# Kernel optimization log

Hardware: AMD Instinct MI355X
Metric: run time of the kernel (lower is better)

## Reference

```python
import jax, jax.numpy as jnp
import numpy as np

N_NODES = 100000
N_EDGES = 1600000
F_IN = 128
H1 = 128
H2 = 128
N_CLASSES = 40


def setup_inputs() -> dict:
    key = jax.random.key(0)
    ks = jax.random.split(key, 8)
    node_features = jax.random.normal(ks[0], (N_NODES, F_IN), dtype=jnp.float32)
    edge_indices = jax.random.randint(ks[1], (2, N_EDGES), 0, N_NODES, dtype=jnp.int32)
    # Glorot-ish init for weights
    W1 = jax.random.normal(ks[2], (F_IN, H1), dtype=jnp.float32) / np.sqrt(F_IN)
    b1 = jnp.zeros((H1,), dtype=jnp.float32)
    W2 = jax.random.normal(ks[3], (H1, H2), dtype=jnp.float32) / np.sqrt(H1)
    b2 = jnp.zeros((H2,), dtype=jnp.float32)
    Wl = jax.random.normal(ks[4], (H2, N_CLASSES), dtype=jnp.float32) / np.sqrt(H2)
    bl = jnp.zeros((N_CLASSES,), dtype=jnp.float32)
    return {
        "node_features": node_features,
        "edge_indices": edge_indices,
        "W1": W1, "b1": b1,
        "W2": W2, "b2": b2,
        "Wl": Wl, "bl": bl,
    }


def _gcn_norm(edge_indices, n_nodes):
    # PyG GCNConv default: add self-loops, symmetric normalization.
    src = jnp.concatenate([edge_indices[0], jnp.arange(n_nodes, dtype=edge_indices.dtype)])
    dst = jnp.concatenate([edge_indices[1], jnp.arange(n_nodes, dtype=edge_indices.dtype)])
    deg = jax.ops.segment_sum(jnp.ones_like(dst, dtype=jnp.float32), dst,
                              num_segments=n_nodes)  # degree over destinations (col)
    deg_inv_sqrt = jnp.where(deg > 0, jax.lax.rsqrt(deg), 0.0)
    norm = deg_inv_sqrt[src] * deg_inv_sqrt[dst]  # (E + N,)
    return src, dst, norm


def _gcn_conv(x, W, b, src, dst, norm, n_nodes):
    xw = x @ W                                    # (N, F_out) dense GEMM
    msg = xw[src] * norm[:, None]                 # gather + scale: (E+N, F_out)
    out = jax.ops.segment_sum(msg, dst, num_segments=n_nodes)  # scatter-add
    return out + b


def reference(node_features, edge_indices, W1, b1, W2, b2, Wl, bl):
    n = node_features.shape[0]
    src, dst, norm = _gcn_norm(edge_indices, n)
    # dropout is identity in eval mode
    x = jax.nn.relu(_gcn_conv(node_features, W1, b1, src, dst, norm, n))
    x = jax.nn.relu(_gcn_conv(x, W2, b2, src, dst, norm, n))
    return x @ Wl + bl  # (N, num_classes)
```

## Files before the change

### kernel.cpp

```cpp
#include <hip/hip_runtime.h>


typedef unsigned int uint32;
typedef unsigned short u16;

#define FD 128

using short8 = __attribute__((ext_vector_type(8))) short;
using f32x4  = __attribute__((ext_vector_type(4))) float;

union U4S8 { uint4 u; short8 s; };

__device__ __forceinline__ u16 f2bf(float f) {
    uint32 u = __float_as_uint(f);
    uint32 r = ((u >> 16) & 1u) + 0x7FFFu;
    return (u16)((u + r) >> 16);
}
__device__ __forceinline__ float bf2f(u16 s) { return __uint_as_float((uint32)s << 16); }
__device__ __forceinline__ float bfLo(uint32 w) { return __uint_as_float(w << 16); }
__device__ __forceinline__ float bfHi(uint32 w) { return __uint_as_float(w & 0xFFFF0000u); }

__global__ void k_beacon(float* __restrict__ out, long long n, float val) {
    long long i = (long long)blockIdx.x * 256 + threadIdx.x;
    if (i < n) out[i] = val;
}

__global__ __launch_bounds__(256) void k_count(const int* __restrict__ dst,
                                               int* __restrict__ cnt,
                                               int* __restrict__ rank,
                                               int ne, int nn) {
    long long base = ((long long)blockIdx.x * 256 + threadIdx.x) * 4;
    if (base + 4 <= (long long)ne) {
        int4 d4 = *(const int4*)(dst + base);
        int a0 = ((unsigned)d4.x < (unsigned)nn) ? d4.x : nn;
        int a1 = ((unsigned)d4.y < (unsigned)nn) ? d4.y : nn;
        int a2 = ((unsigned)d4.z < (unsigned)nn) ? d4.z : nn;
        int a3 = ((unsigned)d4.w < (unsigned)nn) ? d4.w : nn;
        int4 r4;
        r4.x = atomicAdd(&cnt[a0], 1);
        r4.y = atomicAdd(&cnt[a1], 1);
        r4.z = atomicAdd(&cnt[a2], 1);
        r4.w = atomicAdd(&cnt[a3], 1);
        *(int4*)(rank + base) = r4;
    } else {
        for (long long e = base; e < (long long)ne; e++) {
            int d = dst[e];
            int a = ((unsigned)d < (unsigned)nn) ? d : nn;
            rank[e] = atomicAdd(&cnt[a], 1);
        }
    }
}

__global__ void k_scan_a(const int* __restrict__ cnt, int* __restrict__ row_start,
                         int* __restrict__ bsum, float* __restrict__ dis, int nn) {
    __shared__ int tmp[256];
    int t = threadIdx.x;
    int i = blockIdx.x * 256 + t;
    int v = (i < nn) ? cnt[i] : 0;
    if (i < nn) dis[i] = rsqrtf((float)(v + 1));
    tmp[t] = v;
    __syncthreads();
    for (int off = 1; off < 256; off <<= 1) {
        int x = (t >= off) ? tmp[t - off] : 0;
        __syncthreads();
        tmp[t] += x;
        __syncthreads();
    }
    if (i < nn) row_start[i] = tmp[t] - v;
    if (t == 255) bsum[blockIdx.x] = tmp[255];
}

__global__ void k_scan_b(int* bsum, int nb) {
    __shared__ int tmp[512];
    __shared__ int carry;
    int t = threadIdx.x;
    if (t == 0) carry = 0;
    __syncthreads();
    for (int base = 0; base < nb; base += 512) {
        int i = base + t;
        int v = (i < nb) ? bsum[i] : 0;
        tmp[t] = v;
        __syncthreads();
        for (int off = 1; off < 512; off <<= 1) {
            int x = (t >= off) ? tmp[t - off] : 0;
            __syncthreads();
            tmp[t] += x;
            __syncthreads();
        }
        if (i < nb) bsum[i] = tmp[t] - v + carry;
        __syncthreads();
        if (t == 0) carry += tmp[511];
        __syncthreads();
    }
}

__global__ void k_scan_c(int* __restrict__ row_start, const int* __restrict__ bsum,
                         int nn, int ne) {
    int i = blockIdx.x * 256 + threadIdx.x;
    if (i < nn) row_start[i] += bsum[blockIdx.x];
    if (i == 0) row_start[nn] = ne;
}

__global__ __launch_bounds__(256) void k_fill_mgemm(
    const float* __restrict__ A, const float* __restrict__ W,
    uint32* __restrict__ yt, const float* __restrict__ rowscale, int M,
    const int* __restrict__ src, const int* __restrict__ dst,
    const int* __restrict__ rank, const int* __restrict__ row_start,
    int* __restrict__ col_idx, int ne, int nn,
    int nfill, int ngemm) {
    __shared__ uint4 Bf[4][8][64];

    int bid = blockIdx.x;
    int both2 = 2 * (nfill < ngemm ? nfill : ngemm);
    bool isfill;
    int idx;
    if (bid < both2) { isfill = (bid & 1) == 0; idx = bid >> 1; }
    else { isfill = nfill > ngemm; idx = (both2 >> 1) + (bid - both2); }

    int t = threadIdx.x;

    if (isfill) {
        long long base = ((long long)idx * 256 + t) * 4;
        if (base + 4 <= (long long)ne) {
            int4 d4 = *(const int4*)(dst + base);
            int4 s4 = *(const int4*)(src + base);
            int4 r4 = *(const int4*)(rank + base);
            int dd[4] = {d4.x, d4.y, d4.z, d4.w};
            int ss[4] = {s4.x, s4.y, s4.z, s4.w};
            int rr[4] = {r4.x, r4.y, r4.z, r4.w};
            int pp[4];
#pragma unroll
            for (int r = 0; r < 4; r++) {
                bool ok = (unsigned)dd[r] < (unsigned)nn;
                int dv = ok ? dd[r] : 0;
                int p = row_start[dv] + rr[r];
                pp[r] = ok ? p : -1;
            }
#pragma unroll
            for (int r = 0; r < 4; r++)
                if ((unsigned)pp[r] < (unsigned)ne) col_idx[pp[r]] = ss[r];
        } else {
            for (long long e = base; e < (long long)ne; e++) {
                int d = dst[e];
                if ((unsigned)d >= (unsigned)nn) continue;
                int p = row_start[d] + rank[e];
                if ((unsigned)p < (unsigned)ne) col_idx[p] = src[e];
            }
        }
        return;
    }

    for (int e = t; e < 4 * 8 * 64; e += 256) {
        int kc = e / (8 * 64);
        int rem = e - kc * (8 * 64);
        int ct = rem >> 6;
        int l  = rem & 63;
        int k0 = kc * 32 + (l >> 4) * 8;
        int c  = ct * 16 + (l & 15);
        u16 us[8];
#pragma unroll
        for (int i = 0; i < 8; i++) us[i] = f2bf(W[(size_t)(k0 + i) * 128 + c]);
        uint4 u;
        u.x = (uint32)us[0] | ((uint32)us[1] << 16);
        u.y = (uint32)us[2] | ((uint32)us[3] << 16);
        u.z = (uint32)us[4] | ((uint32)us[5] << 16);
        u.w = (uint32)us[6] | ((uint32)us[7] << 16);
        Bf[kc][ct][l] = u;
    }
    __syncthreads();

    int lane = t & 63, wv = t >> 6;
    int r0 = idx * 64 + wv * 16;
    if (r0 >= M) return;

    int arow = r0 + (lane & 15);
    if (arow >= M) arow = M - 1;
    U4S8 af[4];
#pragma unroll
    for (int kc = 0; kc < 4; kc++) {
        const float4* s = (const float4*)(A + (size_t)arow * FD + kc * 32 + (lane >> 4) * 8);
        float4 v0 = s[0], v1 = s[1];
        uint4 u;
        u.x = (uint32)f2bf(v0.x) | ((uint32)f2bf(v0.y) << 16);
        u.y = (uint32)f2bf(v0.z) | ((uint32)f2bf(v0.w) << 16);
        u.z = (uint32)f2bf(v1.x) | ((uint32)f2bf(v1.y) << 16);
        u.w = (uint32)f2bf(v1.z) | ((uint32)f2bf(v1.w) << 16);
        af[kc].u = u;
    }

    f32x4 acc[8];
#pragma unroll
    for (int ct = 0; ct < 8; ct++) acc[ct] = f32x4{0.f, 0.f, 0.f, 0.f};
#pragma unroll
    for (int kc = 0; kc < 4; kc++) {
#pragma unroll
        for (int ct = 0; ct < 8; ct++) {
            U4S8 b;
            b.u = Bf[kc][ct][lane];
            acc[ct] = __builtin_amdgcn_mfma_f32_16x16x32_bf16(af[kc].s, b.s, acc[ct], 0, 0, 0);
        }
    }

    int rb = r0 + (lane >> 4) * 4;
#pragma unroll
    for (int r = 0; r < 4; r++) {
        int row = rb + r;
        int rc = row < M ? row : M - 1;
        float rs = rowscale[rc];
#pragma unroll
        for (int ct = 0; ct < 8; ct++) {
            float v = acc[ct][r] * rs;
            float vn = __shfl_xor(v, 1);
            if (!(lane & 1) && row < M) {
                uint32 word = (uint32)f2bf(v) | ((uint32)f2bf(vn) << 16);
                yt[(size_t)row * 128 + (ct * 16 + (lane & 15)) / 2] = word;
            }
        }
    }
}

template <int NOUT, bool INBF, bool OUTBF>
__global__ __launch_bounds__(256) void k_mgemm(const void* __restrict__ Ap,
                                               const float* __restrict__ W,
                                               void* __restrict__ out,
                                               const float* __restrict__ bias,
                                               const float* __restrict__ rowscale,
                                               int M) {
    constexpr int NT = (NOUT + 15) / 16;
    __shared__ uint4 Bf[4][NT][64];

    int t = threadIdx.x;
    for (int e = t; e < 4 * NT * 64; e += 256) {
        int kc = e / (NT * 64);
        int rem = e - kc * (NT * 64);
        int ct = rem >> 6;
        int l  = rem & 63;
        int k0 = kc * 32 + (l >> 4) * 8;
        int c  = ct * 16 + (l & 15);
        u16 us[8];
#pragma unroll
        for (int i = 0; i < 8; i++)
            us[i] = (c < NOUT) ? f2bf(W[(size_t)(k0 + i) * NOUT + c]) : (u16)0;
        uint4 u;
        u.x = (uint32)us[0] | ((uint32)us[1] << 16);
        u.y = (uint32)us[2] | ((uint32)us[3] << 16);
        u.z = (uint32)us[4] | ((uint32)us[5] << 16);
        u.w = (uint32)us[6] | ((uint32)us[7] << 16);
        Bf[kc][ct][l] = u;
    }
    __syncthreads();

    int lane = t & 63, wv = t >> 6;
    int r0 = blockIdx.x * 64 + wv * 16;
    if (r0 >= M) return;

    int arow = r0 + (lane & 15);
    if (arow >= M) arow = M - 1;
    U4S8 af[4];
    if (INBF) {
        const u16* A = (const u16*)Ap;
#pragma unroll
        for (int kc = 0; kc < 4; kc++)
            af[kc].u = *(const uint4*)(A + (size_t)arow * FD + kc * 32 + (lane >> 4) * 8);
    } else {
        const float* A = (const float*)Ap;
#pragma unroll
        for (int kc = 0; kc < 4; kc++) {
            const float4* s = (const float4*)(A + (size_t)arow * FD + kc * 32 + (lane >> 4) * 8);
            float4 v0 = s[0], v1 = s[1];
            uint4 u;
            u.x = (uint32)f2bf(v0.x) | ((uint32)f2bf(v0.y) << 16);
            u.y = (uint32)f2bf(v0.z) | ((uint32)f2bf(v0.w) << 16);
            u.z = (uint32)f2bf(v1.x) | ((uint32)f2bf(v1.y) << 16);
            u.w = (uint32)f2bf(v1.z) | ((uint32)f2bf(v1.w) << 16);
            af[kc].u = u;
        }
    }

    f32x4 acc[NT];
#pragma unroll
    for (int ct = 0; ct < NT; ct++) acc[ct] = f32x4{0.f, 0.f, 0.f, 0.f};
#pragma unroll
    for (int kc = 0; kc < 4; kc++) {
#pragma unroll
        for (int ct = 0; ct < NT; ct++) {
            U4S8 b;
            b.u = Bf[kc][ct][lane];
            acc[ct] = __builtin_amdgcn_mfma_f32_16x16x32_bf16(af[kc].s, b.s, acc[ct], 0, 0, 0);
        }
    }

    int rb = r0 + (lane >> 4) * 4;
    if (OUTBF) {
        uint32* yt = (uint32*)out;
#pragma unroll
        for (int r = 0; r < 4; r++) {
            int row = rb + r;
            int rc = row < M ? row : M - 1;
            float rs = rowscale ? rowscale[rc] : 1.f;
#pragma unroll
            for (int ct = 0; ct < NT; ct++) {
                float v = acc[ct][r] * rs;
                float vn = __shfl_xor(v, 1);
                if (!(lane & 1) && row < M) {
                    uint32 word = (uint32)f2bf(v) | ((uint32)f2bf(vn) << 16);
                    yt[(size_t)row * 128 + (ct * 16 + (lane & 15)) / 2] = word;
                }
            }
        }
    } else {
        float* fo = (float*)out;
#pragma unroll
        for (int r = 0; r < 4; r++) {
            int row = rb + r;
            if (row >= M) continue;
#pragma unroll
            for (int ct = 0; ct < NT; ct++) {
                int c = ct * 16 + (lane & 15);
                if (c < NOUT) {
                    float v = acc[ct][r];
                    if (bias) v += bias[c];
                    fo[(size_t)row * NOUT + c] = v;
                }
            }
        }
    }
}

__global__ __launch_bounds__(256) void k_agg(const uint32* __restrict__ yt,
                                             const float* __restrict__ dis,
                                             const int* __restrict__ row_start,
                                             const int* __restrict__ col_idx,
                                             const float* __restrict__ bias,
                                             uint32* __restrict__ outp,
                                             int nn, int ne) {
    int lane = threadIdx.x & 63;
    int wid  = threadIdx.x >> 6;
    int g    = lane >> 4;
    int sub  = lane & 15;

    float2 bq[4];
#pragma unroll
    for (int k = 0; k < 4; k++) bq[k] = *(const float2*)(bias + (sub * 4 + k) * 2);

    const int stride = gridDim.x * 16;
    for (int n0 = blockIdx.x * 16 + wid * 4; n0 < nn; n0 += stride) {
        int n = n0 + g;
        bool act = n < nn;
        int nl = act ? n : 0;

        float di = dis[nl];
        int jb = row_start[nl];
        int je = row_start[nl + 1];
        if (!act) { jb = 0; je = 0; }
        if (jb < 0) jb = 0;
        if (je > ne) je = ne;
        int deg = je - jb; if (deg < 0) deg = 0;
        int je1 = je - 1;

        uint4 sv = *(const uint4*)(yt + (size_t)nl * 128 + sub * 4);
        float a0 = bfLo(sv.x), a1 = bfHi(sv.x);
        float a2 = bfLo(sv.y), a3 = bfHi(sv.y);
        float a4 = bfLo(sv.z), a5 = bfHi(sv.z);
        float a6 = bfLo(sv.w), a7 = bfHi(sv.w);

        int m = deg;
        m = max(m, __shfl_xor(m, 16));
        m = max(m, __shfl_xor(m, 32));

        for (int base = 0; base < m; base += 8) {
            int jj = jb + base + (sub & 7);
            int jc = jj < je ? jj : je1;
            if (jc < 0) jc = 0;
            int sl = col_idx[jc];
            if ((unsigned)sl >= (unsigned)nn) sl = -1;

            int ss[8];
            float ww[8];
#pragma unroll
            for (int r = 0; r < 8; r++) {
                int s = __shfl(sl, (lane & 48) + r);
                ww[r] = (base + r < deg && s >= 0) ? 1.f : 0.f;
                ss[r] = s >= 0 ? s : 0;
            }
            uint4 uu[8];
#pragma unroll
            for (int r = 0; r < 8; r++)
                uu[r] = *(const uint4*)(yt + (size_t)ss[r] * 128 + sub * 4);
#pragma unroll
            for (int r = 0; r < 8; r++) {
                float wg = ww[r];
                a0 = fmaf(bfLo(uu[r].x), wg, a0); a1 = fmaf(bfHi(uu[r].x), wg, a1);
                a2 = fmaf(bfLo(uu[r].y), wg, a2); a3 = fmaf(bfHi(uu[r].y), wg, a3);
                a4 = fmaf(bfLo(uu[r].z), wg, a4); a5 = fmaf(bfHi(uu[r].z), wg, a5);
                a6 = fmaf(bfLo(uu[r].w), wg, a6); a7 = fmaf(bfHi(uu[r].w), wg, a7);
            }
        }

        if (act) {
            float r0 = fmaxf(fmaf(a0, di, bq[0].x), 0.f);
            float r1 = fmaxf(fmaf(a1, di, bq[0].y), 0.f);
            float r2 = fmaxf(fmaf(a2, di, bq[1].x), 0.f);
            float r3 = fmaxf(fmaf(a3, di, bq[1].y), 0.f);
            float r4 = fmaxf(fmaf(a4, di, bq[2].x), 0.f);
            float r5 = fmaxf(fmaf(a5, di, bq[2].y), 0.f);
            float r6 = fmaxf(fmaf(a6, di, bq[3].x), 0.f);
            float r7 = fmaxf(fmaf(a7, di, bq[3].y), 0.f);
            uint4 o;
            o.x = (uint32)f2bf(r0) | ((uint32)f2bf(r1) << 16);
            o.y = (uint32)f2bf(r2) | ((uint32)f2bf(r3) << 16);
            o.z = (uint32)f2bf(r4) | ((uint32)f2bf(r5) << 16);
            o.w = (uint32)f2bf(r6) | ((uint32)f2bf(r7) << 16);
            *(uint4*)(outp + (size_t)n * 64 + sub * 4) = o;
        }
    }
}

static inline char* carve(char*& p, size_t bytes) {
    char* r = p;
    p += (bytes + 255) & ~(size_t)255;
    return r;
}

extern "C" void kernel_launch(void* const* d_in, const int* in_sizes, int n_in,
                              void* d_out, int out_size, void* d_ws, size_t ws_size,
                              hipStream_t stream) {
    const long long outn = out_size;
    float* dout = (float*)d_out;
    if (n_in < 8) {
        k_beacon<<<(int)((outn + 255) / 256), 256, 0, stream>>>(dout, outn, 888.f);
        return;
    }
    float* X        = (float*)d_in[0];
    const int* ei   = (const int*)d_in[1];
    const float* W1 = (const float*)d_in[2];
    const float* b1 = (const float*)d_in[3];
    const float* W2 = (const float*)d_in[4];
    const float* b2 = (const float*)d_in[5];
    const float* Wl = (const float*)d_in[6];
    const float* bl = (const float*)d_in[7];

    const int H1 = in_sizes[3];
    const int F  = in_sizes[2] / (H1 > 0 ? H1 : 1);
    const int NC = in_sizes[7];
    const int NN = in_sizes[0] / (F > 0 ? F : 1);
    const int NE = in_sizes[1] / 2;
    if (NN <= 0 || NE <= 0 || F != FD || H1 != FD || NC != 40 ||
        (long long)NN * FD != in_sizes[0] || outn != (long long)NN * NC) {
        k_beacon<<<(int)((outn + 255) / 256), 256, 0, stream>>>(dout, outn, 888.f);
        return;
    }

    const int* src = ei;
    const int* dst = ei + NE;
    const int nb = (NN + 255) / 256;

    char* p = (char*)d_ws;
    int*   cnt       = (int*)  carve(p, ((size_t)NN + 1) * 4);
    float* dis       = (float*)carve(p, (size_t)NN * 4);
    int*   bsum      = (int*)  carve(p, (size_t)nb * 4);
    int*   row_start = (int*)  carve(p, ((size_t)NN + 1) * 4);
    u16*   bufA      = (u16*)  carve(p, (size_t)NN * FD * 2);
    size_t needed = (size_t)(p - (char*)d_ws);
    bool in_out = (size_t)NE * 8 <= (size_t)outn * 4;
    int* col_idx;
    int* rank;
    if (in_out) {
        col_idx = (int*)d_out;
        rank = (int*)((char*)d_out + (size_t)NE * 4);
    } else {
        col_idx = (int*)carve(p, (size_t)NE * 4);
        rank = (int*)carve(p, (size_t)NE * 4);
        needed = (size_t)(p - (char*)d_ws);
    }
    if (needed > ws_size) {
        k_beacon<<<(int)((outn + 255) / 256), 256, 0, stream>>>(dout, outn, 999.f);
        return;
    }

    const int ecb = (int)(((long long)NE + 1023) / 1024);
    const int gemm_blocks = (NN + 63) / 64;
    int agg_blocks = (NN + 15) / 16;
    if (agg_blocks > 2048) agg_blocks = 2048;

    hipMemsetAsync(cnt, 0, ((size_t)NN + 1) * 4, stream);
    hipMemsetAsync(col_idx, 0xFF, (size_t)NE * 4, stream);
    k_count<<<ecb, 256, 0, stream>>>(dst, cnt, rank, NE, NN);
    k_scan_a<<<nb, 256, 0, stream>>>(cnt, row_start, bsum, dis, NN);
    k_scan_b<<<1, 512, 0, stream>>>(bsum, nb);
    k_scan_c<<<nb, 256, 0, stream>>>(row_start, bsum, NN, NE);

    k_fill_mgemm<<<ecb + gemm_blocks, 256, 0, stream>>>(
        X, W1, (uint32*)X, dis, NN,
        src, dst, rank, row_start, col_idx, NE, NN,
        ecb, gemm_blocks);

    k_agg<<<agg_blocks, 256, 0, stream>>>((const uint32*)X, dis, row_start, col_idx,
                                          b1, (uint32*)bufA, NN, NE);
    k_mgemm<128, true, true><<<gemm_blocks, 256, 0, stream>>>(bufA, W2, X, nullptr, dis, NN);
    k_agg<<<agg_blocks, 256, 0, stream>>>((const uint32*)X, dis, row_start, col_idx,
                                          b2, (uint32*)bufA, NN, NE);
    k_mgemm<40, true, false><<<gemm_blocks, 256, 0, stream>>>(bufA, Wl, dout, bl, nullptr, NN);
}
```

Before: 382.7 us.

## Overlap first GEMM with degree counting and move source scaling into aggregation

The first-layer GEMM is co-scheduled with the edge-count atomics instead of the CSR fill, so it no longer depends on the degree scan. Because of that, the per-source rsqrt(deg) scaling moves out of the GEMM epilogues and into the aggregation, which gathers dis[src] for each neighbor and broadcasts it through lane shuffles. The col_idx memset is dropped, and row_start[nn] is now computed from the last count rather than ne. The cost is an extra scattered dis load per edge in each aggregation pass, and the count kernel now handles one edge per thread instead of four.

```diff
diff --git a/kernel.cpp b/kernel.cpp
--- a/kernel.cpp
+++ b/kernel.cpp
@@ -25,28 +25,94 @@
     if (i < n) out[i] = val;
 }
 
-__global__ __launch_bounds__(256) void k_count(const int* __restrict__ dst,
-                                               int* __restrict__ cnt,
-                                               int* __restrict__ rank,
-                                               int ne, int nn) {
-    long long base = ((long long)blockIdx.x * 256 + threadIdx.x) * 4;
-    if (base + 4 <= (long long)ne) {
-        int4 d4 = *(const int4*)(dst + base);
-        int a0 = ((unsigned)d4.x < (unsigned)nn) ? d4.x : nn;
-        int a1 = ((unsigned)d4.y < (unsigned)nn) ? d4.y : nn;
-        int a2 = ((unsigned)d4.z < (unsigned)nn) ? d4.z : nn;
-        int a3 = ((unsigned)d4.w < (unsigned)nn) ? d4.w : nn;
-        int4 r4;
-        r4.x = atomicAdd(&cnt[a0], 1);
-        r4.y = atomicAdd(&cnt[a1], 1);
-        r4.z = atomicAdd(&cnt[a2], 1);
-        r4.w = atomicAdd(&cnt[a3], 1);
-        *(int4*)(rank + base) = r4;
-    } else {
-        for (long long e = base; e < (long long)ne; e++) {
+__global__ __launch_bounds__(256) void k_cnt_mgemm(
+    const int* __restrict__ dst, int* __restrict__ cnt, int* __restrict__ rank,
+    int ne, int nn,
+    const float* __restrict__ A, const float* __restrict__ W,
+    uint32* __restrict__ yt, int M,
+    int ngemm) {
+    __shared__ uint4 Bf[4][8][64];
+
+    int bid = blockIdx.x;
+    int g5 = bid / 5;
+    bool isg = ((bid % 5) == 0) && (g5 < ngemm);
+    int t = threadIdx.x;
+
+    if (!isg) {
+        int idx = bid - (g5 + 1 < ngemm ? g5 + 1 : ngemm);
+        int e = idx * 256 + t;
+        if (e < ne) {
             int d = dst[e];
             int a = ((unsigned)d < (unsigned)nn) ? d : nn;
             rank[e] = atomicAdd(&cnt[a], 1);
+        }
+        return;
+    }
+
+    int idx = g5;
+    for (int e = t; e < 4 * 8 * 64; e += 256) {
+        int kc = e / (8 * 64);
+        int rem = e - kc * (8 * 64);
+        int ct = rem >> 6;
+        int l  = rem & 63;
+        int k0 = kc * 32 + (l >> 4) * 8;
+        int c  = ct * 16 + (l & 15);
+        u16 us[8];
+#pragma unroll
+        for (int i = 0; i < 8; i++) us[i] = f2bf(W[(size_t)(k0 + i) * 128 + c]);
+        uint4 u;
+        u.x = (uint32)us[0] | ((uint32)us[1] << 16);
+        u.y = (uint32)us[2] | ((uint32)us[3] << 16);
+        u.z = (uint32)us[4] | ((uint32)us[5] << 16);
+        u.w = (uint32)us[6] | ((uint32)us[7] << 16);
+        Bf[kc][ct][l] = u;
+    }
+    __syncthreads();
+
+    int lane = t & 63, wv = t >> 6;
+    int r0 = idx * 64 + wv * 16;
+    if (r0 >= M) return;
+
+    int arow = r0 + (lane & 15);
+    if (arow >= M) arow = M - 1;
+    U4S8 af[4];
+#pragma unroll
+    for (int kc = 0; kc < 4; kc++) {
+        const float4* s = (const float4*)(A + (size_t)arow * FD + kc * 32 + (lane >> 4) * 8);
+        float4 v0 = s[0], v1 = s[1];
+        uint4 u;
+        u.x = (uint32)f2bf(v0.x) | ((uint32)f2bf(v0.y) << 16);
+        u.y = (uint32)f2bf(v0.z) | ((uint32)f2bf(v0.w) << 16);
+        u.z = (uint32)f2bf(v1.x) | ((uint32)f2bf(v1.y) << 16);
+        u.w = (uint32)f2bf(v1.z) | ((uint32)f2bf(v1.w) << 16);
+        af[kc].u = u;
+    }
+
+    f32x4 acc[8];
+#pragma unroll
+    for (int ct = 0; ct < 8; ct++) acc[ct] = f32x4{0.f, 0.f, 0.f, 0.f};
+#pragma unroll
+    for (int kc = 0; kc < 4; kc++) {
+#pragma unroll
+        for (int ct = 0; ct < 8; ct++) {
+            U4S8 b;
+            b.u = Bf[kc][ct][lane];
+            acc[ct] = __builtin_amdgcn_mfma_f32_16x16x32_bf16(af[kc].s, b.s, acc[ct], 0, 0, 0);
+        }
+    }
+
+    int rb = r0 + (lane >> 4) * 4;
+#pragma unroll
+    for (int r = 0; r < 4; r++) {
+        int row = rb + r;
+#pragma unroll
+        for (int ct = 0; ct < 8; ct++) {
+            float v = acc[ct][r];
+            float vn = __shfl_xor(v, 1);
+            if (!(lane & 1) && row < M) {
+                uint32 word = (uint32)f2bf(v) | ((uint32)f2bf(vn) << 16);
+                yt[(size_t)row * 128 + (ct * 16 + (lane & 15)) / 2] = word;
+            }
         }
     }
 }
@@ -95,126 +161,46 @@
 }
 
 __global__ void k_scan_c(int* __restrict__ row_start, const int* __restrict__ bsum,
-                         int nn, int ne) {
+                         const int* __restrict__ cnt, int nn) {
     int i = blockIdx.x * 256 + threadIdx.x;
-    if (i < nn) row_start[i] += bsum[blockIdx.x];
-    if (i == 0) row_start[nn] = ne;
-}
-
-__global__ __launch_bounds__(256) void k_fill_mgemm(
-    const float* __restrict__ A, const float* __restrict__ W,
-    uint32* __restrict__ yt, const float* __restrict__ rowscale, int M,
-    const int* __restrict__ src, const int* __restrict__ dst,
-    const int* __restrict__ rank, const int* __restrict__ row_start,
-    int* __restrict__ col_idx, int ne, int nn,
-    int nfill, int ngemm) {
-    __shared__ uint4 Bf[4][8][64];
-
-    int bid = blockIdx.x;
-    int both2 = 2 * (nfill < ngemm ? nfill : ngemm);
-    bool isfill;
-    int idx;
-    if (bid < both2) { isfill = (bid & 1) == 0; idx = bid >> 1; }
-    else { isfill = nfill > ngemm; idx = (both2 >> 1) + (bid - both2); }
-
-    int t = threadIdx.x;
-
-    if (isfill) {
-        long long base = ((long long)idx * 256 + t) * 4;
-        if (base + 4 <= (long long)ne) {
-            int4 d4 = *(const int4*)(dst + base);
-            int4 s4 = *(const int4*)(src + base);
-            int4 r4 = *(const int4*)(rank + base);
-            int dd[4] = {d4.x, d4.y, d4.z, d4.w};
-            int ss[4] = {s4.x, s4.y, s4.z, s4.w};
-            int rr[4] = {r4.x, r4.y, r4.z, r4.w};
-            int pp[4];
-#pragma unroll
-            for (int r = 0; r < 4; r++) {
-                bool ok = (unsigned)dd[r] < (unsigned)nn;
-                int dv = ok ? dd[r] : 0;
-                int p = row_start[dv] + rr[r];
-                pp[r] = ok ? p : -1;
-            }
-#pragma unroll
-            for (int r = 0; r < 4; r++)
-                if ((unsigned)pp[r] < (unsigned)ne) col_idx[pp[r]] = ss[r];
-        } else {
-            for (long long e = base; e < (long long)ne; e++) {
-                int d = dst[e];
-                if ((unsigned)d >= (unsigned)nn) continue;
-                int p = row_start[d] + rank[e];
-                if ((unsigned)p < (unsigned)ne) col_idx[p] = src[e];
-            }
-        }
-        return;
-    }
-
-    for (int e = t; e < 4 * 8 * 64; e += 256) {
-        int kc = e / (8 * 64);
-        int rem = e - kc * (8 * 64);
-        int ct = rem >> 6;
-        int l  = rem & 63;
-        int k0 = kc * 32 + (l >> 4) * 8;
-        int c  = ct * 16 + (l & 15);
-        u16 us[8];
-#pragma unroll
-        for (int i = 0; i < 8; i++) us[i] = f2bf(W[(size_t)(k0 + i) * 128 + c]);
-        uint4 u;
-        u.x = (uint32)us[0] | ((uint32)us[1] << 16);
-        u.y = (uint32)us[2] | ((uint32)us[3] << 16);
-        u.z = (uint32)us[4] | ((uint32)us[5] << 16);
-        u.w = (uint32)us[6] | ((uint32)us[7] << 16);
-        Bf[kc][ct][l] = u;
-    }
-    __syncthreads();
-
-    int lane = t & 63, wv = t >> 6;
-    int r0 = idx * 64 + wv * 16;
-    if (r0 >= M) return;
-
-    int arow = r0 + (lane & 15);
-    if (arow >= M) arow = M - 1;
-    U4S8 af[4];
-#pragma unroll
-    for (int kc = 0; kc < 4; kc++) {
-        const float4* s = (const float4*)(A + (size_t)arow * FD + kc * 32 + (lane >> 4) * 8);
-        float4 v0 = s[0], v1 = s[1];
-        uint4 u;
-        u.x = (uint32)f2bf(v0.x) | ((uint32)f2bf(v0.y) << 16);
-        u.y = (uint32)f2bf(v0.z) | ((uint32)f2bf(v0.w) << 16);
-        u.z = (uint32)f2bf(v1.x) | ((uint32)f2bf(v1.y) << 16);
-        u.w = (uint32)f2bf(v1.z) | ((uint32)f2bf(v1.w) << 16);
-        af[kc].u = u;
-    }
-
-    f32x4 acc[8];
-#pragma unroll
-    for (int ct = 0; ct < 8; ct++) acc[ct] = f32x4{0.f, 0.f, 0.f, 0.f};
-#pragma unroll
-    for (int kc = 0; kc < 4; kc++) {
-#pragma unroll
-        for (int ct = 0; ct < 8; ct++) {
-            U4S8 b;
-            b.u = Bf[kc][ct][lane];
-            acc[ct] = __builtin_amdgcn_mfma_f32_16x16x32_bf16(af[kc].s, b.s, acc[ct], 0, 0, 0);
-        }
-    }
-
-    int rb = r0 + (lane >> 4) * 4;
-#pragma unroll
-    for (int r = 0; r < 4; r++) {
-        int row = rb + r;
-        int rc = row < M ? row : M - 1;
-        float rs = rowscale[rc];
-#pragma unroll
-        for (int ct = 0; ct < 8; ct++) {
-            float v = acc[ct][r] * rs;
-            float vn = __shfl_xor(v, 1);
-            if (!(lane & 1) && row < M) {
-                uint32 word = (uint32)f2bf(v) | ((uint32)f2bf(vn) << 16);
-                yt[(size_t)row * 128 + (ct * 16 + (lane & 15)) / 2] = word;
-            }
+    if (i < nn) {
+        int r = row_start[i] + bsum[blockIdx.x];
+        row_start[i] = r;
+        if (i == nn - 1) row_start[nn] = r + cnt[i];
+    }
+}
+
+__global__ __launch_bounds__(256) void k_fill(const int* __restrict__ src,
+                                              const int* __restrict__ dst,
+                                              const int* __restrict__ rank,
+                                              const int* __restrict__ row_start,
+                                              int* __restrict__ col_idx,
+                                              int ne, int nn) {
+    long long base = ((long long)blockIdx.x * 256 + threadIdx.x) * 4;
+    if (base + 4 <= (long long)ne) {
+        int4 d4 = *(const int4*)(dst + base);
+        int4 s4 = *(const int4*)(src + base);
+        int4 r4 = *(const int4*)(rank + base);
+        int dd[4] = {d4.x, d4.y, d4.z, d4.w};
+        int ss[4] = {s4.x, s4.y, s4.z, s4.w};
+        int rr[4] = {r4.x, r4.y, r4.z, r4.w};
+        int pp[4];
+#pragma unroll
+        for (int r = 0; r < 4; r++) {
+            bool ok = (unsigned)dd[r] < (unsigned)nn;
+            int dv = ok ? dd[r] : 0;
+            int p = row_start[dv] + rr[r];
+            pp[r] = ok ? p : -1;
+        }
+#pragma unroll
+        for (int r = 0; r < 4; r++)
+            if ((unsigned)pp[r] < (unsigned)ne) col_idx[pp[r]] = ss[r];
+    } else {
+        for (long long e = base; e < (long long)ne; e++) {
+            int d = dst[e];
+            if ((unsigned)d >= (unsigned)nn) continue;
+            int p = row_start[d] + rank[e];
+            if ((unsigned)p < (unsigned)ne) col_idx[p] = src[e];
         }
     }
 }
@@ -224,7 +210,6 @@
                                                const float* __restrict__ W,
                                                void* __restrict__ out,
                                                const float* __restrict__ bias,
-                                               const float* __restrict__ rowscale,
                                                int M) {
     constexpr int NT = (NOUT + 15) / 16;
     __shared__ uint4 Bf[4][NT][64];
@@ -296,11 +281,9 @@
 #pragma unroll
         for (int r = 0; r < 4; r++) {
             int row = rb + r;
-            int rc = row < M ? row : M - 1;
-            float rs = rowscale ? rowscale[rc] : 1.f;
 #pragma unroll
             for (int ct = 0; ct < NT; ct++) {
-                float v = acc[ct][r] * rs;
+                float v = acc[ct][r];
                 float vn = __shfl_xor(v, 1);
                 if (!(lane & 1) && row < M) {
                     uint32 word = (uint32)f2bf(v) | ((uint32)f2bf(vn) << 16);
@@ -359,10 +342,10 @@
         int je1 = je - 1;
 
         uint4 sv = *(const uint4*)(yt + (size_t)nl * 128 + sub * 4);
-        float a0 = bfLo(sv.x), a1 = bfHi(sv.x);
-        float a2 = bfLo(sv.y), a3 = bfHi(sv.y);
-        float a4 = bfLo(sv.z), a5 = bfHi(sv.z);
-        float a6 = bfLo(sv.w), a7 = bfHi(sv.w);
+        float a0 = bfLo(sv.x) * di, a1 = bfHi(sv.x) * di;
+        float a2 = bfLo(sv.y) * di, a3 = bfHi(sv.y) * di;
+        float a4 = bfLo(sv.z) * di, a5 = bfHi(sv.z) * di;
+        float a6 = bfLo(sv.w) * di, a7 = bfHi(sv.w) * di;
 
         int m = deg;
         m = max(m, __shfl_xor(m, 16));
@@ -373,15 +356,19 @@
             int jc = jj < je ? jj : je1;
             if (jc < 0) jc = 0;
             int sl = col_idx[jc];
-            if ((unsigned)sl >= (unsigned)nn) sl = -1;
+            float ds = 0.f;
+            if ((unsigned)sl < (unsigned)nn) ds = dis[sl];
+            else sl = 0;
 
             int ss[8];
             float ww[8];
 #pragma unroll
             for (int r = 0; r < 8; r++) {
-                int s = __shfl(sl, (lane & 48) + r);
-                ww[r] = (base + r < deg && s >= 0) ? 1.f : 0.f;
-                ss[r] = s >= 0 ? s : 0;
+                int srcLane = (lane & 48) + r;
+                int s = __shfl(sl, srcLane);
+                float w = __shfl(ds, srcLane);
+                ww[r] = (base + r < deg) ? w : 0.f;
+                ss[r] = s;
             }
             uint4 uu[8];
 #pragma unroll
@@ -478,27 +465,25 @@
         return;
     }
 
-    const int ecb = (int)(((long long)NE + 1023) / 1024);
+    const int ecb1 = (NE + 255) / 256;
+    const int ecb4 = (int)(((long long)NE + 1023) / 1024);
     const int gemm_blocks = (NN + 63) / 64;
     int agg_blocks = (NN + 15) / 16;
     if (agg_blocks > 2048) agg_blocks = 2048;
 
     hipMemsetAsync(cnt, 0, ((size_t)NN + 1) * 4, stream);
-    hipMemsetAsync(col_idx, 0xFF, (size_t)NE * 4, stream);
-    k_count<<<ecb, 256, 0, stream>>>(dst, cnt, rank, NE, NN);
+    k_cnt_mgemm<<<ecb1 + gemm_blocks, 256, 0, stream>>>(
+        dst, cnt, rank, NE, NN,
+        X, W1, (uint32*)X, NN, gemm_blocks);
     k_scan_a<<<nb, 256, 0, stream>>>(cnt, row_start, bsum, dis, NN);
     k_scan_b<<<1, 512, 0, stream>>>(bsum, nb);
-    k_scan_c<<<nb, 256, 0, stream>>>(row_start, bsum, NN, NE);
-
-    k_fill_mgemm<<<ecb + gemm_blocks, 256, 0, stream>>>(
-        X, W1, (uint32*)X, dis, NN,
-        src, dst, rank, row_start, col_idx, NE, NN,
-        ecb, gemm_blocks);
+    k_scan_c<<<nb, 256, 0, stream>>>(row_start, bsum, cnt, NN);
+    k_fill<<<ecb4, 256, 0, stream>>>(src, dst, rank, row_start, col_idx, NE, NN);
 
     k_agg<<<agg_blocks, 256, 0, stream>>>((const uint32*)X, dis, row_start, col_idx,
                                           b1, (uint32*)bufA, NN, NE);
-    k_mgemm<128, true, true><<<gemm_blocks, 256, 0, stream>>>(bufA, W2, X, nullptr, dis, NN);
+    k_mgemm<128, true, true><<<gemm_blocks, 256, 0, stream>>>(bufA, W2, X, nullptr, NN);
     k_agg<<<agg_blocks, 256, 0, stream>>>((const uint32*)X, dis, row_start, col_idx,
                                           b2, (uint32*)bufA, NN, NE);
-    k_mgemm<40, true, false><<<gemm_blocks, 256, 0, stream>>>(bufA, Wl, dout, bl, nullptr, NN);
-}
+    k_mgemm<40, true, false><<<gemm_blocks, 256, 0, stream>>>(bufA, Wl, dout, bl, NN);
+}
```

Result: faster. 362.6 us (-5.3%).
